# Kernel optimization log

Measured on AMD Instinct MI355X. Metric: run time of the kernel, lower is better.

The kernel has to match this reference:

```python
import jax, jax.numpy as jnp
import numpy as np
from jax import lax

N_HEADS = 8
D_K = 64
D_V = 64
TEMP = float(np.sqrt(D_K))  # MixtureOfSoftMax temperature = d_k ** 0.5


def avg_pool_3x3_s2_same(x):
    """TF-style AveragePooling2D(pool=3, stride=2, padding='same'), NHWC.
    TF excludes padded elements from the average (divide by valid count)."""
    sums = lax.reduce_window(x, 0.0, lax.add, (1, 3, 3, 1), (1, 2, 2, 1), 'SAME')
    ones = jnp.ones(x.shape[:3] + (1,), x.dtype)
    cnt = lax.reduce_window(ones, 0.0, lax.add, (1, 3, 3, 1), (1, 2, 2, 1), 'SAME')
    return sums / cnt


def conv1x1(x, w, b):
    # 1x1 conv == per-pixel channel matmul
    return jnp.einsum('bhwc,cd->bhwd', x, w) + b


def setup_inputs() -> dict:
    key = jax.random.key(0)
    ks = jax.random.split(key, 6)
    C = 512
    s1 = float(np.sqrt(2.0 / (C + D_K)))  # init_weight1 std
    s3 = float(np.sqrt(2.0 / (C + D_V)))  # init_weight3 std
    return {
        'x':   jax.random.normal(ks[0], (4, 64, 64, C), jnp.float32),
        'w_q': jax.random.normal(ks[1], (C, N_HEADS * D_K), jnp.float32) * s1,
        'b_q': jnp.zeros((N_HEADS * D_K,), jnp.float32),
        'w_k': jax.random.normal(ks[2], (C, N_HEADS * D_K), jnp.float32) * s1,
        'b_k': jnp.zeros((N_HEADS * D_K,), jnp.float32),
        'w_v': jax.random.normal(ks[3], (C, N_HEADS * D_V), jnp.float32) * s3,
        'b_v': jnp.zeros((N_HEADS * D_V,), jnp.float32),
        'w_o': jax.random.normal(ks[4], (N_HEADS * D_V, C), jnp.float32) * 0.02,
        'b_o': jnp.zeros((C,), jnp.float32),
    }


def reference(x, w_q, b_q, w_k, b_k, w_v, b_v, w_o, b_o):
    BS, H, W, C = x.shape
    residual = x
    # Q from full-res x; K, V from 3x3/s2 average-pooled x (pooling=True)
    qt = conv1x1(x, w_q, b_q).reshape(BS * N_HEADS, H * W, -1)          # (B*h, N, d_k)
    xp = avg_pool_3x3_s2_same(x)                                         # (BS, H/2, W/2, C)
    kt = conv1x1(xp, w_k, b_k).reshape(BS * N_HEADS, H * W // 4, -1)     # (B*h, N/4, d_k)
    vt = conv1x1(xp, w_v, b_v).reshape(BS * N_HEADS, H * W // 4, -1)     # (B*h, N/4, d_v)
    # MixtureOfSoftMaxACF with n_mix=1: scaled dot-product softmax attention
    attn = jnp.einsum('bnd,bmd->bnm', qt, kt) / TEMP                     # (B*h, N, N/4)
    attn = jax.nn.softmax(attn, axis=-1)                                 # dropout=identity (inference)
    out = jnp.einsum('bnm,bmd->bnd', attn, vt)                           # (B*h, N, d_v)
    out = out.reshape(BS, H, W, -1)
    out = conv1x1(out, w_o, b_o)                                         # conv1x1_bn_relu (Conv2D only in call)
    return out + residual                                                # concat=False -> Add
```

## Files before the change

### kernel.cpp

```cpp
#include <hip/hip_runtime.h>
#include <hip/hip_bf16.h>
#include <math.h>

typedef short bf16x8 __attribute__((ext_vector_type(8)));
typedef float f32x4 __attribute__((ext_vector_type(4)));
typedef unsigned short u16;

__device__ inline float b2f(u16 h) {
    unsigned int u = ((unsigned int)h) << 16;
    float f;
    __builtin_memcpy(&f, &u, 4);
    return f;
}

__device__ inline u16 f2b(float f) {
    unsigned int u;
    __builtin_memcpy(&u, &f, 4);
    unsigned int lsb = (u >> 16) & 1u;
    u += 0x7fffu + lsb;
    return (u16)(u >> 16);
}

__device__ __forceinline__ void gl2lds16(const u16* g, u16* l) {
    __builtin_amdgcn_global_load_lds(
        (const __attribute__((address_space(1))) unsigned int*)g,
        (__attribute__((address_space(3))) unsigned int*)l,
        16, 0, 0);
}

#define PITCH 72

#define QSCALE 0.18033688011112042f

__global__ __launch_bounds__(256) void cvtw_kernel(const float* __restrict__ x,
                                                   u16* __restrict__ xb,
                                                   const float* __restrict__ w0,
                                                   const float* __restrict__ w1,
                                                   const float* __restrict__ w2,
                                                   const float* __restrict__ w3,
                                                   u16* __restrict__ wt) {
    __shared__ u16 T[64 * PITCH];
    int tid = threadIdx.x;
    if (blockIdx.x < 8192) {
        int idx = blockIdx.x * 256 + tid;
        float4 v = ((const float4*)x)[idx];
        ushort4 o;
        o.x = f2b(v.x); o.y = f2b(v.y); o.z = f2b(v.z); o.w = f2b(v.w);
        ((ushort4*)xb)[idx] = o;
        return;
    }
    int t5 = blockIdx.x - 8192;
    int bx = t5 & 7, by = (t5 >> 3) & 7, bz = t5 >> 6;
    const float* W = bz == 0 ? w0 : bz == 1 ? w1 : bz == 2 ? w2 : w3;
    u16* WT = wt + (size_t)bz * 262144;
    int nB = bx * 64, kB = by * 64;
#pragma unroll
    for (int t = 0; t < 4; ++t) {
        int e = tid + t * 256;
        int r = e >> 4, c4 = (e & 15) * 4;
        float4 v = *(const float4*)(&W[(size_t)(kB + r) * 512 + nB + c4]);
        u16* dst = &T[r * PITCH + c4];
        dst[0] = f2b(v.x); dst[1] = f2b(v.y); dst[2] = f2b(v.z); dst[3] = f2b(v.w);
    }
    __syncthreads();
    int n = tid & 63, kg = tid >> 6;
#pragma unroll
    for (int p = 0; p < 2; ++p) {
        int k0 = (kg + p * 4) * 8;
        u16 tmp[8];
#pragma unroll
        for (int i = 0; i < 8; ++i) tmp[i] = T[(k0 + i) * PITCH + n];
        *(int4*)(&WT[(size_t)(nB + n) * 512 + kB + k0]) = *(int4*)tmp;
    }
}

__device__ __forceinline__ void pool_body(int idx, const u16* __restrict__ xb,
                                          u16* __restrict__ xp) {
    int c8 = idx & 63;
    int j = (idx >> 6) & 31;
    int i = (idx >> 11) & 31;
    int b = idx >> 16;
    int r0 = 2 * i, c0 = 2 * j;
    int rmax = min(r0 + 3, 64), cmax = min(c0 + 3, 64);
    float acc[8] = {};
    for (int r = r0; r < rmax; ++r)
        for (int cc = c0; cc < cmax; ++cc) {
            bf16x8 v = *(const bf16x8*)(
                &xb[(size_t)((((b << 6) + r) << 6) + cc) * 512 + c8 * 8]);
#pragma unroll
            for (int t = 0; t < 8; ++t) acc[t] += b2f(((const u16*)&v)[t]);
        }
    float inv = 1.f / (float)((rmax - r0) * (cmax - c0));
    u16 o[8];
#pragma unroll
    for (int t = 0; t < 8; ++t) o[t] = f2b(acc[t] * inv);
    *(int4*)(&xp[(size_t)idx * 8]) = *(int4*)o;
}

template <int OM, int BN, int GY>
__device__ __forceinline__ void gemm_body(int bid,
                                          const u16* __restrict__ A,
                                          const u16* __restrict__ WT,
                                          const float* __restrict__ bias,
                                          const float* __restrict__ bias2res,
                                          void* __restrict__ Cv,
                                          void* __restrict__ Cv2,
                                          float oscale,
                                          u16* At, u16* Bt) {
    int tid = threadIdx.x, lane = tid & 63, wave = tid >> 6;
    int q = lane >> 4, l16 = lane & 15;
    constexpr int MI = (BN == 128) ? 2 : 1;
    int wm, wn;
    if constexpr (BN == 128) { wm = wave & 1; wn = wave >> 1; }
    else                     { wm = wave;     wn = 0; }
    int nBlk = bid / GY;
    int mBlk = bid - nBlk * GY;
    int nBase = nBlk * BN, mBase = mBlk * 64;
    f32x4 acc[MI][4] = {};

    for (int kk = 0; kk < 512; kk += 64) {
        __syncthreads();
#pragma unroll
        for (int t = 0; t < 2; ++t) {
            int c = tid + t * 256;
            int m = c >> 3, kc = (c & 7) ^ (m & 7);
            gl2lds16(&A[(size_t)(mBase + m) * 512 + kk + kc * 8], &At[c * 8]);
        }
#pragma unroll
        for (int t = 0; t < BN / 32; ++t) {
            int c = tid + t * 256;
            int m = c >> 3, kc = (c & 7) ^ (m & 7);
            gl2lds16(&WT[(size_t)(nBase + m) * 512 + kk + kc * 8], &Bt[c * 8]);
        }
        __syncthreads();
#pragma unroll
        for (int ds = 0; ds < 2; ++ds) {
            bf16x8 a[MI], b[4];
#pragma unroll
            for (int i = 0; i < MI; ++i) {
                int ma = (BN == 128 ? wm * 32 : wm * 16) + i * 16 + l16;
                a[i] = *(bf16x8*)(&At[ma * 64 + ((((ds << 2) + q) ^ (ma & 7)) << 3)]);
            }
#pragma unroll
            for (int j = 0; j < 4; ++j) {
                int nb = wn * 64 + j * 16 + l16;
                b[j] = *(bf16x8*)(&Bt[nb * 64 + ((((ds << 2) + q) ^ (nb & 7)) << 3)]);
            }
#pragma unroll
            for (int i = 0; i < MI; ++i)
#pragma unroll
                for (int j = 0; j < 4; ++j)
                    acc[i][j] = __builtin_amdgcn_mfma_f32_16x16x32_bf16(a[i], b[j], acc[i][j], 0, 0, 0);
        }
    }

    bool isK = (OM != 3) || (nBase < 512);
#pragma unroll
    for (int j = 0; j < 4; ++j) {
        int col = nBase + wn * 64 + j * 16 + l16;
        float bv;
        if constexpr (OM == 3) bv = isK ? bias[col] : bias2res[col - 512];
        else bv = bias[col];
#pragma unroll
        for (int i = 0; i < MI; ++i) {
#pragma unroll
            for (int r = 0; r < 4; ++r) {
                int row = mBase + (BN == 128 ? wm * 32 : wm * 16) + i * 16 + q * 4 + r;
                float v = acc[i][j][r] + bv;
                if constexpr (OM == 1) {
                    v += bias2res[(size_t)row * 512 + col];
                    ((float*)Cv)[(size_t)row * 512 + col] = v;
                } else if constexpr (OM == 0) {
                    ((u16*)Cv)[(size_t)row * 512 + col] = f2b(v * oscale);
                } else {
                    if (isK) {
                        ((u16*)Cv)[(size_t)row * 512 + col] = f2b(v);
                    } else {
                        int colv = col - 512;
                        int g = row >> 7, m2 = ((row & 127) << 3) + (colv >> 6), d = colv & 63;
                        ((u16*)Cv2)[(size_t)((g << 6) + d) * 1024 + m2] = f2b(v);
                    }
                }
            }
        }
    }
}

__global__ __launch_bounds__(256, 4) void qpool_kernel(const u16* __restrict__ xb,
                                                       const u16* __restrict__ wTq,
                                                       const float* __restrict__ b_q,
                                                       u16* __restrict__ Qw,
                                                       u16* __restrict__ xp) {
    __shared__ __align__(16) u16 At[64 * 64];
    __shared__ __align__(16) u16 Bt[128 * 64];
    int gid = blockIdx.x;
    if (gid < 1024) {
        gemm_body<0, 128, 256>(gid, xb, wTq, b_q, nullptr, Qw, nullptr, QSCALE, At, Bt);
    } else {
        pool_body((gid - 1024) * 256 + threadIdx.x, xb, xp);
    }
}

__global__ __launch_bounds__(256, 4) void gemm_kv_kernel(const u16* __restrict__ xp,
                                                         const u16* __restrict__ wTkv,
                                                         const float* __restrict__ b_k,
                                                         const float* __restrict__ b_v,
                                                         u16* __restrict__ Kw,
                                                         u16* __restrict__ VwT) {
    __shared__ __align__(16) u16 At[64 * 64];
    __shared__ __align__(16) u16 Bt[64 * 64];
    gemm_body<3, 64, 64>(blockIdx.x, xp, wTkv, b_k, b_v, Kw, VwT, 1.0f, At, Bt);
}

__global__ __launch_bounds__(256, 4) void gemm_o_kernel(const u16* __restrict__ Ow,
                                                        const u16* __restrict__ wTo,
                                                        const float* __restrict__ b_o,
                                                        const float* __restrict__ xres,
                                                        float* __restrict__ out) {
    __shared__ __align__(16) u16 At[64 * 64];
    __shared__ __align__(16) u16 Bt[128 * 64];
    gemm_body<1, 128, 256>(blockIdx.x, Ow, wTo, b_o, xres, out, nullptr, 1.0f, At, Bt);
}

__global__ __launch_bounds__(256, 4) void attn_kernel(const u16* __restrict__ Q,
                                                      const u16* __restrict__ K,
                                                      const u16* __restrict__ VT_g,
                                                      u16* __restrict__ O) {
    int g = blockIdx.x;
    int qtile = blockIdx.y;
    const u16* Qg = Q + (size_t)g * 262144;
    const u16* Kg = K + (size_t)g * 65536;
    const u16* Vt = VT_g + (size_t)g * 65536;
    u16* Og = O + (size_t)g * 262144;

    __shared__ __align__(16) u16 Kt[128 * 64];
    __shared__ __align__(16) u16 VTs[64 * 128];
    __shared__ __align__(16) u16 Pt[64 * 64];

    int tid = threadIdx.x, lane = tid & 63, wave = tid >> 6;
    int q = lane >> 4, l16 = lane & 15;
    int n0 = qtile * 128;
    int pkey = (l16 & 7) << 2;
    int prow = (wave * 16 + l16) * 32;
    int* Pt32 = (int*)Pt;

    bf16x8 qf[2][2];
#pragma unroll
    for (int s = 0; s < 2; ++s)
#pragma unroll
        for (int ds = 0; ds < 2; ++ds)
            qf[s][ds] = *(const bf16x8*)(
                &Qg[(size_t)(n0 + s * 64 + wave * 16 + l16) * 64 + ds * 32 + q * 8]);

    f32x4 oacc[2][4] = {};
    float rsum[2] = {0.f, 0.f};

    for (int kb = 0; kb < 8; ++kb) {
        __syncthreads();
#pragma unroll
        for (int t = 0; t < 4; ++t) {
            int c = wave * 64 + lane + t * 256;
            {
                int m = c >> 3, kc = (c & 7) ^ (m & 7);
                gl2lds16(&Kg[(size_t)(kb * 128 + m) * 64 + kc * 8], &Kt[c * 8]);
            }
            {
                int d = c >> 4, mc = (c & 15) ^ (d & 15);
                gl2lds16(&Vt[(size_t)d * 1024 + kb * 128 + mc * 8], &VTs[c * 8]);
            }
        }
        __syncthreads();

#pragma unroll
        for (int h = 0; h < 2; ++h) {
#pragma unroll
            for (int s = 0; s < 2; ++s) {
#pragma unroll
                for (int cb = 0; cb < 4; ++cb) {
                    int m = h * 64 + cb * 16 + l16;
                    bf16x8 kf0 = *(bf16x8*)(&Kt[m * 64 + ((q ^ (m & 7)) << 3)]);
                    bf16x8 kf1 = *(bf16x8*)(&Kt[m * 64 + (((4 + q) ^ (m & 7)) << 3)]);
                    f32x4 z = {};
                    __builtin_amdgcn_s_setprio(1);
                    z = __builtin_amdgcn_mfma_f32_16x16x32_bf16(kf0, qf[s][0], z, 0, 0, 0);
                    z = __builtin_amdgcn_mfma_f32_16x16x32_bf16(kf1, qf[s][1], z, 0, 0, 0);
                    __builtin_amdgcn_s_setprio(0);
                    float p0 = __builtin_amdgcn_exp2f(z[0]);
                    float p1 = __builtin_amdgcn_exp2f(z[1]);
                    float p2 = __builtin_amdgcn_exp2f(z[2]);
                    float p3 = __builtin_amdgcn_exp2f(z[3]);
                    rsum[s] += (p0 + p1) + (p2 + p3);
                    unsigned w0, w1;
                    asm("v_cvt_pk_bf16_f32 %0, %1, %2" : "=v"(w0) : "v"(p0), "v"(p1));
                    asm("v_cvt_pk_bf16_f32 %0, %1, %2" : "=v"(w1) : "v"(p2), "v"(p3));
                    int2 w;
                    w.x = (int)w0;
                    w.y = (int)w1;
                    int pd = (cb * 8 + q * 2) ^ pkey;
                    *(int2*)(&Pt32[prow + pd]) = w;
                }
#pragma unroll
                for (int ds = 0; ds < 2; ++ds) {
                    int pd = (ds * 16 + q * 4) ^ pkey;
                    bf16x8 ap = *(bf16x8*)(&Pt32[prow + pd]);
                    __builtin_amdgcn_s_setprio(1);
#pragma unroll
                    for (int db = 0; db < 4; ++db) {
                        int dd = db * 16 + l16;
                        int jj = h * 8 + ds * 4 + q;
                        bf16x8 vb = *(bf16x8*)(&VTs[dd * 128 + ((jj ^ (dd & 15)) << 3)]);
                        oacc[s][db] = __builtin_amdgcn_mfma_f32_16x16x32_bf16(ap, vb, oacc[s][db], 0, 0, 0);
                    }
                    __builtin_amdgcn_s_setprio(0);
                }
            }
        }
    }

#pragma unroll
    for (int s = 0; s < 2; ++s) {
        float v = rsum[s];
        v += __shfl_xor(v, 16, 64);
        v += __shfl_xor(v, 32, 64);
        rsum[s] = v;
    }
    float inv[2][4];
#pragma unroll
    for (int s = 0; s < 2; ++s)
#pragma unroll
        for (int r = 0; r < 4; ++r)
            inv[s][r] = 1.f / __shfl(rsum[s], q * 4 + r, 64);
#pragma unroll
    for (int s = 0; s < 2; ++s)
#pragma unroll
        for (int db = 0; db < 4; ++db)
#pragma unroll
            for (int r = 0; r < 4; ++r) {
                int row = n0 + s * 64 + wave * 16 + q * 4 + r;
                Og[(size_t)row * 64 + db * 16 + l16] = f2b(oacc[s][db][r] * inv[s][r]);
            }
}

extern "C" void kernel_launch(void* const* d_in, const int* in_sizes, int n_in,
                              void* d_out, int out_size, void* d_ws, size_t ws_size,
                              hipStream_t stream) {
    const float* x   = (const float*)d_in[0];
    const float* w_q = (const float*)d_in[1];
    const float* b_q = (const float*)d_in[2];
    const float* w_k = (const float*)d_in[3];
    const float* b_k = (const float*)d_in[4];
    const float* w_v = (const float*)d_in[5];
    const float* b_v = (const float*)d_in[6];
    const float* w_o = (const float*)d_in[7];
    const float* b_o = (const float*)d_in[8];
    float* out = (float*)d_out;

    char* ws = (char*)d_ws;
    u16* xb  = (u16*)(ws);
    u16* xp  = (u16*)(ws + (16ull << 20));
    u16* Qw  = (u16*)(ws + (20ull << 20));
    u16* Kw  = (u16*)(ws + (36ull << 20));
    u16* VwT = (u16*)(ws + (40ull << 20));
    u16* wT  = (u16*)(ws + (44ull << 20));
    u16* Ow  = xb;

    cvtw_kernel<<<8448, 256, 0, stream>>>(x, xb, w_q, w_k, w_v, w_o, wT);
    qpool_kernel<<<2048, 256, 0, stream>>>(xb, wT, b_q, Qw, xp);
    gemm_kv_kernel<<<1024, 256, 0, stream>>>(xp, wT + 262144, b_k, b_v, Kw, VwT);
    attn_kernel<<<dim3(32, 32), 256, 0, stream>>>(Qw, Kw, VwT, Ow);
    gemm_o_kernel<<<1024, 256, 0, stream>>>(Ow, wT + 786432, b_o, x, out);
}
```

Baseline: 196.8 us.

## Double-buffer LDS tiles in projection GEMMs to overlap loads with MFMA

```diff
diff --git a/kernel.cpp b/kernel.cpp
--- a/kernel.cpp
+++ b/kernel.cpp
@@ -118,33 +118,38 @@
     int nBase = nBlk * BN, mBase = mBlk * 64;
     f32x4 acc[MI][4] = {};
 
-    for (int kk = 0; kk < 512; kk += 64) {
-        __syncthreads();
+    auto stage = [&](int buf, int kk) {
+        u16* Ab = At + buf * (64 * 64);
+        u16* Bb = Bt + buf * (BN * 64);
 #pragma unroll
         for (int t = 0; t < 2; ++t) {
             int c = tid + t * 256;
             int m = c >> 3, kc = (c & 7) ^ (m & 7);
-            gl2lds16(&A[(size_t)(mBase + m) * 512 + kk + kc * 8], &At[c * 8]);
+            gl2lds16(&A[(size_t)(mBase + m) * 512 + kk + kc * 8], &Ab[c * 8]);
         }
 #pragma unroll
         for (int t = 0; t < BN / 32; ++t) {
             int c = tid + t * 256;
             int m = c >> 3, kc = (c & 7) ^ (m & 7);
-            gl2lds16(&WT[(size_t)(nBase + m) * 512 + kk + kc * 8], &Bt[c * 8]);
-        }
-        __syncthreads();
+            gl2lds16(&WT[(size_t)(nBase + m) * 512 + kk + kc * 8], &Bb[c * 8]);
+        }
+    };
+
+    auto compute = [&](int buf) {
+        const u16* Ab = At + buf * (64 * 64);
+        const u16* Bb = Bt + buf * (BN * 64);
 #pragma unroll
         for (int ds = 0; ds < 2; ++ds) {
             bf16x8 a[MI], b[4];
 #pragma unroll
             for (int i = 0; i < MI; ++i) {
                 int ma = (BN == 128 ? wm * 32 : wm * 16) + i * 16 + l16;
-                a[i] = *(bf16x8*)(&At[ma * 64 + ((((ds << 2) + q) ^ (ma & 7)) << 3)]);
+                a[i] = *(const bf16x8*)(&Ab[ma * 64 + ((((ds << 2) + q) ^ (ma & 7)) << 3)]);
             }
 #pragma unroll
             for (int j = 0; j < 4; ++j) {
                 int nb = wn * 64 + j * 16 + l16;
-                b[j] = *(bf16x8*)(&Bt[nb * 64 + ((((ds << 2) + q) ^ (nb & 7)) << 3)]);
+                b[j] = *(const bf16x8*)(&Bb[nb * 64 + ((((ds << 2) + q) ^ (nb & 7)) << 3)]);
             }
 #pragma unroll
             for (int i = 0; i < MI; ++i)
@@ -152,7 +157,21 @@
                 for (int j = 0; j < 4; ++j)
                     acc[i][j] = __builtin_amdgcn_mfma_f32_16x16x32_bf16(a[i], b[j], acc[i][j], 0, 0, 0);
         }
-    }
+    };
+
+    stage(0, 0);
+    asm volatile("s_waitcnt vmcnt(0)" ::: "memory");
+    __builtin_amdgcn_s_barrier();
+    int cur = 0;
+#pragma unroll 1
+    for (int kk = 64; kk < 512; kk += 64) {
+        stage(cur ^ 1, kk);
+        compute(cur);
+        asm volatile("s_waitcnt vmcnt(0)" ::: "memory");
+        __builtin_amdgcn_s_barrier();
+        cur ^= 1;
+    }
+    compute(cur);
 
     bool isK = (OM != 3) || (nBase < 512);
 #pragma unroll
@@ -186,13 +205,13 @@
     }
 }
 
-__global__ __launch_bounds__(256, 4) void qpool_kernel(const u16* __restrict__ xb,
+__global__ __launch_bounds__(256, 3) void qpool_kernel(const u16* __restrict__ xb,
                                                        const u16* __restrict__ wTq,
                                                        const float* __restrict__ b_q,
                                                        u16* __restrict__ Qw,
                                                        u16* __restrict__ xp) {
-    __shared__ __align__(16) u16 At[64 * 64];
-    __shared__ __align__(16) u16 Bt[128 * 64];
+    __shared__ __align__(16) u16 At[2 * 64 * 64];
+    __shared__ __align__(16) u16 Bt[2 * 128 * 64];
     int gid = blockIdx.x;
     if (gid < 1024) {
         gemm_body<0, 128, 256>(gid, xb, wTq, b_q, nullptr, Qw, nullptr, QSCALE, At, Bt);
@@ -207,18 +226,18 @@
                                                          const float* __restrict__ b_v,
                                                          u16* __restrict__ Kw,
                                                          u16* __restrict__ VwT) {
-    __shared__ __align__(16) u16 At[64 * 64];
-    __shared__ __align__(16) u16 Bt[64 * 64];
+    __shared__ __align__(16) u16 At[2 * 64 * 64];
+    __shared__ __align__(16) u16 Bt[2 * 64 * 64];
     gemm_body<3, 64, 64>(blockIdx.x, xp, wTkv, b_k, b_v, Kw, VwT, 1.0f, At, Bt);
 }
 
-__global__ __launch_bounds__(256, 4) void gemm_o_kernel(const u16* __restrict__ Ow,
+__global__ __launch_bounds__(256, 3) void gemm_o_kernel(const u16* __restrict__ Ow,
                                                         const u16* __restrict__ wTo,
                                                         const float* __restrict__ b_o,
                                                         const float* __restrict__ xres,
                                                         float* __restrict__ out) {
-    __shared__ __align__(16) u16 At[64 * 64];
-    __shared__ __align__(16) u16 Bt[128 * 64];
+    __shared__ __align__(16) u16 At[2 * 64 * 64];
+    __shared__ __align__(16) u16 Bt[2 * 128 * 64];
     gemm_body<1, 128, 256>(blockIdx.x, Ow, wTo, b_o, xres, out, nullptr, 1.0f, At, Bt);
 }
 
```

New measurement: 202.3 us. +2.8%, slower.

## Double-buffer K/V tiles in attention kernel with 64-key prefetch

Applied to the files above, without the earlier changes.

```diff
diff --git a/kernel.cpp b/kernel.cpp
--- a/kernel.cpp
+++ b/kernel.cpp
@@ -233,8 +233,8 @@
     const u16* Vt = VT_g + (size_t)g * 65536;
     u16* Og = O + (size_t)g * 262144;
 
-    __shared__ __align__(16) u16 Kt[128 * 64];
-    __shared__ __align__(16) u16 VTs[64 * 128];
+    __shared__ __align__(16) u16 Kt[2][64 * 64];
+    __shared__ __align__(16) u16 VTs[2][64 * 64];
     __shared__ __align__(16) u16 Pt[64 * 64];
 
     int tid = threadIdx.x, lane = tid & 63, wave = tid >> 6;
@@ -255,66 +255,70 @@
     f32x4 oacc[2][4] = {};
     float rsum[2] = {0.f, 0.f};
 
-    for (int kb = 0; kb < 8; ++kb) {
+    auto stage = [&](int buf, int kb) {
+#pragma unroll
+        for (int t = 0; t < 2; ++t) {
+            int c = tid + t * 256;
+            int m = c >> 3, kc = (c & 7) ^ (m & 7);
+            gl2lds16(&Kg[(size_t)(kb * 64 + m) * 64 + kc * 8], &Kt[buf][c * 8]);
+            gl2lds16(&Vt[(size_t)m * 1024 + kb * 64 + kc * 8], &VTs[buf][c * 8]);
+        }
+    };
+
+    stage(0, 0);
+    asm volatile("s_waitcnt vmcnt(0)" ::: "memory");
+    __syncthreads();
+
+    int cur = 0;
+#pragma unroll 1
+    for (int kb = 0; kb < 16; ++kb) {
+        if (kb < 15) stage(cur ^ 1, kb + 1);
+        const u16* KtB = Kt[cur];
+        const u16* VTsB = VTs[cur];
+#pragma unroll
+        for (int s = 0; s < 2; ++s) {
+#pragma unroll
+            for (int cb = 0; cb < 4; ++cb) {
+                int m = cb * 16 + l16;
+                bf16x8 kf0 = *(const bf16x8*)(&KtB[m * 64 + ((q ^ (m & 7)) << 3)]);
+                bf16x8 kf1 = *(const bf16x8*)(&KtB[m * 64 + (((4 + q) ^ (m & 7)) << 3)]);
+                f32x4 z = {};
+                __builtin_amdgcn_s_setprio(1);
+                z = __builtin_amdgcn_mfma_f32_16x16x32_bf16(kf0, qf[s][0], z, 0, 0, 0);
+                z = __builtin_amdgcn_mfma_f32_16x16x32_bf16(kf1, qf[s][1], z, 0, 0, 0);
+                __builtin_amdgcn_s_setprio(0);
+                float p0 = __builtin_amdgcn_exp2f(z[0]);
+                float p1 = __builtin_amdgcn_exp2f(z[1]);
+                float p2 = __builtin_amdgcn_exp2f(z[2]);
+                float p3 = __builtin_amdgcn_exp2f(z[3]);
+                rsum[s] += (p0 + p1) + (p2 + p3);
+                unsigned w0, w1;
+                asm("v_cvt_pk_bf16_f32 %0, %1, %2" : "=v"(w0) : "v"(p0), "v"(p1));
+                asm("v_cvt_pk_bf16_f32 %0, %1, %2" : "=v"(w1) : "v"(p2), "v"(p3));
+                int2 w;
+                w.x = (int)w0;
+                w.y = (int)w1;
+                int pd = (cb * 8 + q * 2) ^ pkey;
+                *(int2*)(&Pt32[prow + pd]) = w;
+            }
+#pragma unroll
+            for (int ds = 0; ds < 2; ++ds) {
+                int pd = (ds * 16 + q * 4) ^ pkey;
+                bf16x8 ap = *(bf16x8*)(&Pt32[prow + pd]);
+                __builtin_amdgcn_s_setprio(1);
+#pragma unroll
+                for (int db = 0; db < 4; ++db) {
+                    int dd = db * 16 + l16;
+                    int jj = ds * 4 + q;
+                    bf16x8 vb = *(const bf16x8*)(&VTsB[dd * 64 + ((jj ^ (dd & 7)) << 3)]);
+                    oacc[s][db] = __builtin_amdgcn_mfma_f32_16x16x32_bf16(ap, vb, oacc[s][db], 0, 0, 0);
+                }
+                __builtin_amdgcn_s_setprio(0);
+            }
+        }
+        asm volatile("s_waitcnt vmcnt(0)" ::: "memory");
         __syncthreads();
-#pragma unroll
-        for (int t = 0; t < 4; ++t) {
-            int c = wave * 64 + lane + t * 256;
-            {
-                int m = c >> 3, kc = (c & 7) ^ (m & 7);
-                gl2lds16(&Kg[(size_t)(kb * 128 + m) * 64 + kc * 8], &Kt[c * 8]);
-            }
-            {
-                int d = c >> 4, mc = (c & 15) ^ (d & 15);
-                gl2lds16(&Vt[(size_t)d * 1024 + kb * 128 + mc * 8], &VTs[c * 8]);
-            }
-        }
-        __syncthreads();
-
-#pragma unroll
-        for (int h = 0; h < 2; ++h) {
-#pragma unroll
-            for (int s = 0; s < 2; ++s) {
-#pragma unroll
-                for (int cb = 0; cb < 4; ++cb) {
-                    int m = h * 64 + cb * 16 + l16;
-                    bf16x8 kf0 = *(bf16x8*)(&Kt[m * 64 + ((q ^ (m & 7)) << 3)]);
-                    bf16x8 kf1 = *(bf16x8*)(&Kt[m * 64 + (((4 + q) ^ (m & 7)) << 3)]);
-                    f32x4 z = {};
-                    __builtin_amdgcn_s_setprio(1);
-                    z = __builtin_amdgcn_mfma_f32_16x16x32_bf16(kf0, qf[s][0], z, 0, 0, 0);
-                    z = __builtin_amdgcn_mfma_f32_16x16x32_bf16(kf1, qf[s][1], z, 0, 0, 0);
-                    __builtin_amdgcn_s_setprio(0);
-                    float p0 = __builtin_amdgcn_exp2f(z[0]);
-                    float p1 = __builtin_amdgcn_exp2f(z[1]);
-                    float p2 = __builtin_amdgcn_exp2f(z[2]);
-                    float p3 = __builtin_amdgcn_exp2f(z[3]);
-                    rsum[s] += (p0 + p1) + (p2 + p3);
-                    unsigned w0, w1;
-                    asm("v_cvt_pk_bf16_f32 %0, %1, %2" : "=v"(w0) : "v"(p0), "v"(p1));
-                    asm("v_cvt_pk_bf16_f32 %0, %1, %2" : "=v"(w1) : "v"(p2), "v"(p3));
-                    int2 w;
-                    w.x = (int)w0;
-                    w.y = (int)w1;
-                    int pd = (cb * 8 + q * 2) ^ pkey;
-                    *(int2*)(&Pt32[prow + pd]) = w;
-                }
-#pragma unroll
-                for (int ds = 0; ds < 2; ++ds) {
-                    int pd = (ds * 16 + q * 4) ^ pkey;
-                    bf16x8 ap = *(bf16x8*)(&Pt32[prow + pd]);
-                    __builtin_amdgcn_s_setprio(1);
-#pragma unroll
-                    for (int db = 0; db < 4; ++db) {
-                        int dd = db * 16 + l16;
-                        int jj = h * 8 + ds * 4 + q;
-                        bf16x8 vb = *(bf16x8*)(&VTs[dd * 128 + ((jj ^ (dd & 15)) << 3)]);
-                        oacc[s][db] = __builtin_amdgcn_mfma_f32_16x16x32_bf16(ap, vb, oacc[s][db], 0, 0, 0);
-                    }
-                    __builtin_amdgcn_s_setprio(0);
-                }
-            }
-        }
+        cur ^= 1;
     }
 
 #pragma unroll
```

After: 201.6 us. 1.02x slower.
